# Kernel tuning notes

Measured on AMD Instinct MI355X. Metric: run time of the kernel, lower is better.

Reference implementation:

```python
import jax, jax.numpy as jnp
import numpy as np

N, E = 50000, 400000
DIN, H, EATTR, OUT = 128, 256, 8, 2
BN_EPS = 1e-5


def setup_inputs() -> dict:
    key = jax.random.key(0)
    ks = iter(jax.random.split(key, 64))
    def w(shape, scale=0.05):
        return (jax.random.normal(next(ks), shape, dtype=jnp.float32) * scale)
    inp = {
        "x": jax.random.normal(next(ks), (N, DIN), dtype=jnp.float32),
        "edge_index": jax.random.randint(next(ks), (2, E), 0, N, dtype=jnp.int32),
        "edge_attr": jax.random.normal(next(ks), (E, EATTR), dtype=jnp.float32),
    }
    # two GCN branches, 3 layers each
    dims = [(DIN, H), (H, H), (H, H)]
    for br in (1, 2):
        for li, (di, do) in enumerate(dims, start=1):
            inp[f"W{br}{li}"] = w((di, do))
            inp[f"b{br}{li}"] = jnp.zeros((do,), jnp.float32)
    # shared batchnorms
    for li in (1, 2, 3):
        inp[f"g{li}"] = jnp.ones((H,), jnp.float32)
        inp[f"be{li}"] = jnp.zeros((H,), jnp.float32)
    # edge classifier MLP: 2H+EATTR -> H -> H -> H//2 -> H//4 -> OUT
    cdims = [(2 * H + EATTR, H), (H, H), (H, H // 2), (H // 2, H // 4), (H // 4, OUT)]
    for li, (di, do) in enumerate(cdims, start=1):
        inp[f"Wc{li}"] = w((di, do))
        inp[f"bc{li}"] = jnp.zeros((do,), jnp.float32)
    return inp


def _gcn(h, W, b, src, dst, inv_sqrt_deg, n):
    # PyG GCNConv: x' = D^-1/2 (A + I) D^-1/2 (x W) + b, deg includes self-loop
    hw = h @ W                                    # [N, out]
    norm = inv_sqrt_deg[src] * inv_sqrt_deg[dst]  # [E]
    agg = jax.ops.segment_sum(hw[src] * norm[:, None], dst, num_segments=n)
    agg = agg + hw * (inv_sqrt_deg ** 2)[:, None]  # self-loop contribution
    return agg + b


def _bn_relu(h, g, b):
    m = h.mean(0)
    v = h.var(0)  # biased, as torch BN training-mode normalization
    return jax.nn.relu(g * (h - m) * jax.lax.rsqrt(v + BN_EPS) + b)


def reference(x, edge_index, edge_attr,
              W11, b11, W12, b12, W13, b13,
              W21, b21, W22, b22, W23, b23,
              g1, be1, g2, be2, g3, be3,
              Wc1, bc1, Wc2, bc2, Wc3, bc3, Wc4, bc4, Wc5, bc5):
    n = x.shape[0]
    src, dst = edge_index[0], edge_index[1]
    deg = 1.0 + jax.ops.segment_sum(jnp.ones(src.shape, x.dtype), dst, num_segments=n)
    isd = deg ** -0.5

    def branch(Ws, bs):
        h = x
        for (W, b, g, be) in zip(Ws, bs, (g1, g2, g3), (be1, be2, be3)):
            h = _gcn(h, W, b, src, dst, isd, n)
            h = _bn_relu(h, g, be)  # dropout = identity (eval)
        return h

    h1 = branch((W11, W12, W13), (b11, b12, b13))
    h2 = branch((W21, W22, W23), (b21, b22, b23))
    hc = h1 + h2

    ef = jnp.concatenate([hc[src], hc[dst], edge_attr], axis=1)  # [E, 2H+EATTR]
    h = jax.nn.relu(ef @ Wc1 + bc1)
    h = jax.nn.relu(h @ Wc2 + bc2)
    h = jax.nn.relu(h @ Wc3 + bc3)
    h = jax.nn.relu(h @ Wc4 + bc4)
    return h @ Wc5 + bc5  # [E, OUT]
```

## Files before the change

### kernel.cpp

```cpp
#include <hip/hip_runtime.h>

#define N_NODES 50000
#define N_EDGES 400000
#define EPB     128
#define NB_SCAN 196
#define BN_EPS  1e-5f
#define STAT_BLOCKS 128

typedef __attribute__((ext_vector_type(8))) short s16x8;
typedef __attribute__((ext_vector_type(4))) float f32x4;

__device__ __forceinline__ unsigned short f2bf(float x) {
    unsigned u = __float_as_uint(x);
    return (unsigned short)((u + 0x7fffu + ((u >> 16) & 1u)) >> 16);
}
__device__ __forceinline__ float bf2f(unsigned short b) {
    return __uint_as_float(((unsigned)b) << 16);
}

__device__ __forceinline__ void gload_lds16(const void* g, void* lds) {
    auto gp = reinterpret_cast<const __attribute__((address_space(1))) unsigned int*>(
        reinterpret_cast<uintptr_t>(g));
    auto lp = reinterpret_cast<__attribute__((address_space(3))) unsigned int*>(
        reinterpret_cast<uintptr_t>(lds));
    __builtin_amdgcn_global_load_lds(gp, lp, 16, 0, 0);
}

__global__ void zero_i32(int* p, int n) {
    int i = blockIdx.x * blockDim.x + threadIdx.x;
    if (i < n) p[i] = 0;
}
__global__ void zero_f32(float* p, int n) {
    int i = blockIdx.x * blockDim.x + threadIdx.x;
    if (i < n) p[i] = 0.0f;
}
__global__ void count_deg(const int* __restrict__ dst, int* __restrict__ counts) {
    int e = blockIdx.x * blockDim.x + threadIdx.x;
    if (e < N_EDGES) atomicAdd(&counts[dst[e]], 1);
}
__global__ void isd_kernel(const int* __restrict__ counts, float* __restrict__ isd) {
    int i = blockIdx.x * blockDim.x + threadIdx.x;
    if (i < N_NODES) isd[i] = rsqrtf(1.0f + (float)counts[i]);
}

__global__ __launch_bounds__(256) void scan_reduce(const int* __restrict__ counts,
                                                   int* __restrict__ bsum) {
    __shared__ int sh[256];
    int t = threadIdx.x, b = blockIdx.x;
    int i = b * 256 + t;
    sh[t] = (i < N_NODES) ? counts[i] : 0;
    __syncthreads();
    for (int o = 128; o > 0; o >>= 1) {
        if (t < o) sh[t] += sh[t + o];
        __syncthreads();
    }
    if (t == 0) bsum[b] = sh[0];
}
__global__ __launch_bounds__(256) void scan_tops(const int* __restrict__ bsum,
                                                 int* __restrict__ boff, int nb,
                                                 int* __restrict__ total_out) {
    __shared__ int sh[256];
    int t = threadIdx.x;
    int v = (t < nb) ? bsum[t] : 0;
    sh[t] = v;
    __syncthreads();
    for (int o = 1; o < 256; o <<= 1) {
        int a = (t >= o) ? sh[t - o] : 0;
        __syncthreads();
        sh[t] += a;
        __syncthreads();
    }
    if (t < nb) boff[t] = sh[t] - v;
    if (t == 255) *total_out = sh[255];
}
__global__ __launch_bounds__(256) void scan_final(const int* __restrict__ counts,
                                                  const int* __restrict__ boff,
                                                  int* __restrict__ offsets) {
    __shared__ int sh[256];
    int t = threadIdx.x, b = blockIdx.x;
    int i = b * 256 + t;
    int v = (i < N_NODES) ? counts[i] : 0;
    sh[t] = v;
    __syncthreads();
    for (int o = 1; o < 256; o <<= 1) {
        int a = (t >= o) ? sh[t - o] : 0;
        __syncthreads();
        sh[t] += a;
        __syncthreads();
    }
    if (i < N_NODES) offsets[i] = boff[b] + sh[t] - v;
}

__global__ void fill_csr(const int* __restrict__ src, const int* __restrict__ dst,
                         const float* __restrict__ isd, const int* __restrict__ offsets,
                         int* __restrict__ cursor, int2* __restrict__ pk,
                         int* __restrict__ edstA, int* __restrict__ eorigA) {
    int e = blockIdx.x * blockDim.x + threadIdx.x;
    if (e >= N_EDGES) return;
    int s = src[e], d = dst[e];
    int pos = offsets[d] + atomicAdd(&cursor[d], 1);
    pk[pos] = make_int2(s, __float_as_int(isd[s] * isd[d]));
    edstA[pos] = d;
    eorigA[pos] = e;
}

__global__ void conv_f32_bf16(const float* __restrict__ in, unsigned short* __restrict__ out,
                              int n4) {
    int i = blockIdx.x * blockDim.x + threadIdx.x;
    if (i >= n4) return;
    float4 v = ((const float4*)in)[i];
    unsigned short o0 = f2bf(v.x), o1 = f2bf(v.y), o2 = f2bf(v.z), o3 = f2bf(v.w);
    ((uint2*)out)[i] = make_uint2(((unsigned)o1 << 16) | o0, ((unsigned)o3 << 16) | o2);
}

struct WPack {
    const float* src[11];
    unsigned short* dst[11];
};
__global__ __launch_bounds__(256) void prep_weights(WPack p) {
    const int Ks[11] = {128, 128, 256, 256, 256, 256, 256, 256, 256, 256, 128};
    const int Ns[11] = {256, 256, 256, 256, 256, 256, 256, 256, 256, 128, 64};
    int seg = blockIdx.y;
    int K = Ks[seg], N = Ns[seg];
    int idx = blockIdx.x * 256 + threadIdx.x;
    if (idx >= K * N) return;
    int k = idx / N, n = idx % N;
    p.dst[seg][(size_t)n * K + k] = f2bf(p.src[seg][idx]);
}

template <int BN_T, int OUT_MODE, int RELU, int BIAS, int DUAL>
__global__ __launch_bounds__(256) void gemm_mfma(const unsigned short* __restrict__ A, int lda,
                                                 const unsigned short* __restrict__ Wt,
                                                 const float* __restrict__ bias,
                                                 void* __restrict__ Cout, int ldc,
                                                 int M, int K,
                                                 const unsigned short* __restrict__ A2,
                                                 const unsigned short* __restrict__ Wt2) {
    constexpr int MI = (BN_T == 128) ? 4 : 2;
    constexpr int NI = 4;
    __shared__ __align__(16) short As[128 * 32];
    __shared__ __align__(16) short Bs[BN_T * 32];

    const int tid = threadIdx.x;
    const int l = tid & 63;
    const int wv = tid >> 6;
    const int wrow = (BN_T == 128) ? (wv >> 1) * 64 : wv * 32;
    const int wcol = (BN_T == 128) ? (wv & 1) * 64 : 0;
    const int bm = blockIdx.x * 128;
    int bn, coloff;
    const unsigned short* Ause;
    const unsigned short* Wuse;
    if (DUAL) {
        int half_ = blockIdx.y >> 1;
        bn = (blockIdx.y & 1) * BN_T;
        coloff = half_ * 256;
        Ause = half_ ? A2 : A;
        Wuse = half_ ? Wt2 : Wt;
    } else {
        bn = blockIdx.y * BN_T;
        coloff = 0;
        Ause = A;
        Wuse = Wt;
    }
    const int rsub = l >> 2;
    const int gl = l & 3;

    f32x4 acc[MI][NI] = {};

    for (int k0 = 0; k0 < K; k0 += 32) {
#pragma unroll
        for (int i = 0; i < 2; i++) {
            int lr = wv * 32 + i * 16 + rsub;
            int gr = bm + lr;
            if (gr >= M) gr = M - 1;
            int gsrc = gl ^ ((lr >> 1) & 3);
            gload_lds16(&Ause[(size_t)gr * lda + k0 + gsrc * 8],
                        &As[(wv * 32 + i * 16) * 32]);
        }
#pragma unroll
        for (int i = 0; i < BN_T / 64; i++) {
            int base = (BN_T == 128) ? (wv * 32 + i * 16) : (wv * 16);
            int lr = base + rsub;
            int gsrc = gl ^ ((lr >> 1) & 3);
            gload_lds16(&Wuse[(size_t)(bn + lr) * K + k0 + gsrc * 8],
                        &Bs[base * 32]);
        }
        __syncthreads();

        s16x8 af[MI], bfr[NI];
        const int q = l >> 4;
#pragma unroll
        for (int mi = 0; mi < MI; mi++) {
            int r = wrow + mi * 16 + (l & 15);
            af[mi] = *(const s16x8*)(&As[r * 32 + ((q ^ ((r >> 1) & 3)) << 3)]);
        }
#pragma unroll
        for (int ni = 0; ni < NI; ni++) {
            int r = wcol + ni * 16 + (l & 15);
            bfr[ni] = *(const s16x8*)(&Bs[r * 32 + ((q ^ ((r >> 1) & 3)) << 3)]);
        }
#pragma unroll
        for (int mi = 0; mi < MI; mi++)
#pragma unroll
            for (int ni = 0; ni < NI; ni++)
                acc[mi][ni] = __builtin_amdgcn_mfma_f32_16x16x32_bf16(af[mi], bfr[ni],
                                                                      acc[mi][ni], 0, 0, 0);
        __syncthreads();
    }

#pragma unroll
    for (int mi = 0; mi < MI; mi++) {
#pragma unroll
        for (int ni = 0; ni < NI; ni++) {
            int colB = coloff + bn + wcol + ni * 16 + (l & 15);
            float bv = BIAS ? bias[colB] : 0.0f;
#pragma unroll
            for (int r = 0; r < 4; r++) {
                int row = bm + wrow + mi * 16 + (l >> 4) * 4 + r;
                if (row < M) {
                    float v = acc[mi][ni][r] + bv;
                    if (RELU) v = fmaxf(v, 0.0f);
                    if (OUT_MODE == 1)
                        ((unsigned short*)Cout)[(size_t)row * ldc + colB] = f2bf(v);
                    else
                        ((float*)Cout)[(size_t)row * ldc + colB] = v;
                }
            }
        }
    }
}

__global__ __launch_bounds__(512, 4) void edge_mlp_fused(
    const unsigned short* __restrict__ PQ, const int2* __restrict__ pk,
    const int* __restrict__ edstA, const int* __restrict__ eorigA,
    const float* __restrict__ ea, const float* __restrict__ Wc1e,
    const float* __restrict__ bc1,
    const unsigned short* __restrict__ Wc2t, const float* __restrict__ bc2,
    const unsigned short* __restrict__ Wc3t, const float* __restrict__ bc3,
    const unsigned short* __restrict__ Wc4t, const float* __restrict__ bc4,
    const float* __restrict__ Wc5, const float* __restrict__ bc5,
    float* __restrict__ out) {
    __shared__ __align__(16) short At[EPB * 256];
    __shared__ __align__(16) short Bs[256 * 32];

    const int tid = threadIdx.x;
    const int l = tid & 63;
    const int wv = tid >> 6;
    const int p0 = blockIdx.x * EPB;
    const int lm = l & 15;
    const int q = l >> 4;
    const int rsub = l >> 2;
    const int gl = l & 3;

    {
        const int c0 = l * 4;
        float bi0 = bc1[c0], bi1 = bc1[c0 + 1], bi2 = bc1[c0 + 2], bi3 = bc1[c0 + 3];
        float4 w8[8];
#pragma unroll
        for (int jj = 0; jj < 8; jj++) w8[jj] = *(const float4*)(&Wc1e[jj * 256 + c0]);
        const int g = l >> 1;
        const int sub = (l & 1) * 4;
#pragma unroll 4
        for (int i = 0; i < 16; i++) {
            int row = wv * 16 + i;
            int p = p0 + row;
            int s = pk[p].x;
            int d = edstA[p];
            int eo = eorigA[p];
            union { int2 v; unsigned short u[4]; } Pu, Qu;
            Pu.v = *(const int2*)(&PQ[(size_t)s * 512 + c0]);
            Qu.v = *(const int2*)(&PQ[(size_t)d * 512 + 256 + c0]);
            float v0 = bf2f(Pu.u[0]) + bf2f(Qu.u[0]) + bi0;
            float v1 = bf2f(Pu.u[1]) + bf2f(Qu.u[1]) + bi1;
            float v2 = bf2f(Pu.u[2]) + bf2f(Qu.u[2]) + bi2;
            float v3 = bf2f(Pu.u[3]) + bf2f(Qu.u[3]) + bi3;
#pragma unroll
            for (int jj = 0; jj < 8; jj++) {
                float av = ea[(size_t)eo * 8 + jj];
                v0 = fmaf(av, w8[jj].x, v0);
                v1 = fmaf(av, w8[jj].y, v1);
                v2 = fmaf(av, w8[jj].z, v2);
                v3 = fmaf(av, w8[jj].w, v3);
            }
            unsigned short o0 = f2bf(fmaxf(v0, 0.0f)), o1 = f2bf(fmaxf(v1, 0.0f));
            unsigned short o2 = f2bf(fmaxf(v2, 0.0f)), o3 = f2bf(fmaxf(v3, 0.0f));
            int off = row * 256 + ((g ^ (row & 7)) << 3) + sub;
            *(uint2*)(&At[off]) =
                make_uint2(((unsigned)o1 << 16) | o0, ((unsigned)o3 << 16) | o2);
        }
    }
    __syncthreads();

    {
        const int wrow = (wv >> 2) * 64;
        const int wcol = (wv & 3) * 64;
        f32x4 acc[4][4] = {};
        for (int k0 = 0; k0 < 256; k0 += 32) {
#pragma unroll
            for (int i = 0; i < 2; i++) {
                int lr = wv * 32 + i * 16 + rsub;
                int gsrc = gl ^ ((lr >> 1) & 3);
                gload_lds16(&Wc2t[(size_t)lr * 256 + k0 + gsrc * 8],
                            &Bs[(wv * 32 + i * 16) * 32]);
            }
            __syncthreads();
            s16x8 af[4], bfr[4];
#pragma unroll
            for (int mi = 0; mi < 4; mi++) {
                int r = wrow + mi * 16 + lm;
                int G = (k0 >> 3) + q;
                af[mi] = *(const s16x8*)(&At[r * 256 + ((G ^ (r & 7)) << 3)]);
            }
#pragma unroll
            for (int ni = 0; ni < 4; ni++) {
                int rb = wcol + ni * 16 + lm;
                bfr[ni] = *(const s16x8*)(&Bs[rb * 32 + ((q ^ ((rb >> 1) & 3)) << 3)]);
            }
#pragma unroll
            for (int mi = 0; mi < 4; mi++)
#pragma unroll
                for (int ni = 0; ni < 4; ni++)
                    acc[mi][ni] = __builtin_amdgcn_mfma_f32_16x16x32_bf16(
                        af[mi], bfr[ni], acc[mi][ni], 0, 0, 0);
            __syncthreads();
        }
#pragma unroll
        for (int mi = 0; mi < 4; mi++) {
#pragma unroll
            for (int ni = 0; ni < 4; ni++) {
                int col = wcol + ni * 16 + lm;
                float bv = bc2[col];
#pragma unroll
                for (int r = 0; r < 4; r++) {
                    int row = wrow + mi * 16 + q * 4 + r;
                    At[row * 256 + (((col >> 3) ^ (row & 7)) << 3) + (col & 7)] =
                        (short)f2bf(fmaxf(acc[mi][ni][r] + bv, 0.0f));
                }
            }
        }
    }
    __syncthreads();

    {
        const int wrow = (wv >> 1) * 32;
        const int wcol = (wv & 1) * 64;
        f32x4 acc[2][4] = {};
        for (int k0 = 0; k0 < 256; k0 += 32) {
            {
                int lr = wv * 16 + rsub;
                int gsrc = gl ^ ((lr >> 1) & 3);
                gload_lds16(&Wc3t[(size_t)lr * 256 + k0 + gsrc * 8],
                            &Bs[(wv * 16) * 32]);
            }
            __syncthreads();
            s16x8 af[2], bfr[4];
#pragma unroll
            for (int mi = 0; mi < 2; mi++) {
                int r = wrow + mi * 16 + lm;
                int G = (k0 >> 3) + q;
                af[mi] = *(const s16x8*)(&At[r * 256 + ((G ^ (r & 7)) << 3)]);
            }
#pragma unroll
            for (int ni = 0; ni < 4; ni++) {
                int rb = wcol + ni * 16 + lm;
                bfr[ni] = *(const s16x8*)(&Bs[rb * 32 + ((q ^ ((rb >> 1) & 3)) << 3)]);
            }
#pragma unroll
            for (int mi = 0; mi < 2; mi++)
#pragma unroll
                for (int ni = 0; ni < 4; ni++)
                    acc[mi][ni] = __builtin_amdgcn_mfma_f32_16x16x32_bf16(
                        af[mi], bfr[ni], acc[mi][ni], 0, 0, 0);
            __syncthreads();
        }
#pragma unroll
        for (int mi = 0; mi < 2; mi++) {
#pragma unroll
            for (int ni = 0; ni < 4; ni++) {
                int col = wcol + ni * 16 + lm;
                float bv = bc3[col];
#pragma unroll
                for (int r = 0; r < 4; r++) {
                    int row = wrow + mi * 16 + q * 4 + r;
                    At[row * 128 + (((col >> 3) ^ (row & 7)) << 3) + (col & 7)] =
                        (short)f2bf(fmaxf(acc[mi][ni][r] + bv, 0.0f));
                }
            }
        }
    }
    __syncthreads();

    {
        const int wrow = wv * 16;
        f32x4 acc[4] = {};
        for (int k0 = 0; k0 < 128; k0 += 32) {
            if (wv < 4) {
                int lr = wv * 16 + rsub;
                int gsrc = gl ^ ((lr >> 1) & 3);
                gload_lds16(&Wc4t[(size_t)lr * 128 + k0 + gsrc * 8],
                            &Bs[(wv * 16) * 32]);
            }
            __syncthreads();
            s16x8 af, bfr[4];
            {
                int r = wrow + lm;
                int G = (k0 >> 3) + q;
                af = *(const s16x8*)(&At[r * 128 + ((G ^ (r & 7)) << 3)]);
            }
#pragma unroll
            for (int ni = 0; ni < 4; ni++) {
                int rb = ni * 16 + lm;
                bfr[ni] = *(const s16x8*)(&Bs[rb * 32 + ((q ^ ((rb >> 1) & 3)) << 3)]);
            }
#pragma unroll
            for (int ni = 0; ni < 4; ni++)
                acc[ni] = __builtin_amdgcn_mfma_f32_16x16x32_bf16(af, bfr[ni],
                                                                  acc[ni], 0, 0, 0);
            __syncthreads();
        }
#pragma unroll
        for (int r = 0; r < 4; r++) {
            float pa = 0.f, pb = 0.f;
#pragma unroll
            for (int ni = 0; ni < 4; ni++) {
                int col = ni * 16 + lm;
                float v = fmaxf(acc[ni][r] + bc4[col], 0.0f);
                pa = fmaf(v, Wc5[col * 2 + 0], pa);
                pb = fmaf(v, Wc5[col * 2 + 1], pb);
            }
#pragma unroll
            for (int o = 1; o < 16; o <<= 1) {
                pa += __shfl_xor(pa, o, 64);
                pb += __shfl_xor(pb, o, 64);
            }
            if (lm == 0) {
                int row = wrow + q * 4 + r;
                int eo = eorigA[p0 + row];
                out[(size_t)eo * 2 + 0] = pa + bc5[0];
                out[(size_t)eo * 2 + 1] = pb + bc5[1];
            }
        }
    }
}

__global__ __launch_bounds__(256) void aggregate2(const unsigned short* __restrict__ hwb,
                                                  const float* __restrict__ isd,
                                                  const int* __restrict__ offsets,
                                                  const int2* __restrict__ pk,
                                                  const float* __restrict__ b1,
                                                  const float* __restrict__ b2,
                                                  unsigned short* __restrict__ hagg) {
    int wv = threadIdx.x >> 6, l = threadIdx.x & 63;
    int n = blockIdx.x * 4 + wv;
    int c0 = l * 8;
    float acc[8] = {};
    int e0 = offsets[n], e1 = offsets[n + 1];
    int k = e0;
    for (; k + 2 <= e1; k += 2) {
        int2 p0 = pk[k], p1 = pk[k + 1];
        union { int4 v; unsigned short u[8]; } U0, U1;
        U0.v = *(const int4*)(&hwb[(size_t)p0.x * 512 + c0]);
        U1.v = *(const int4*)(&hwb[(size_t)p1.x * 512 + c0]);
        float w0 = __int_as_float(p0.y), w1 = __int_as_float(p1.y);
#pragma unroll
        for (int j = 0; j < 8; j++)
            acc[j] = fmaf(w0, bf2f(U0.u[j]), fmaf(w1, bf2f(U1.u[j]), acc[j]));
    }
    if (k < e1) {
        int2 p0 = pk[k];
        union { int4 v; unsigned short u[8]; } U0;
        U0.v = *(const int4*)(&hwb[(size_t)p0.x * 512 + c0]);
        float w0 = __int_as_float(p0.y);
#pragma unroll
        for (int j = 0; j < 8; j++) acc[j] = fmaf(w0, bf2f(U0.u[j]), acc[j]);
    }
    float si = isd[n]; si *= si;
    union { int4 v; unsigned short u[8]; } U;
    U.v = *(const int4*)(&hwb[(size_t)n * 512 + c0]);
    const float* bp = (c0 < 256) ? (b1 + c0) : (b2 + (c0 - 256));
    unsigned short os[8];
#pragma unroll
    for (int j = 0; j < 8; j++) {
        acc[j] = fmaf(si, bf2f(U.u[j]), acc[j]) + bp[j];
        os[j] = f2bf(acc[j]);
    }
    int4 ov;
    ov.x = (int)(((unsigned)os[1] << 16) | os[0]);
    ov.y = (int)(((unsigned)os[3] << 16) | os[2]);
    ov.z = (int)(((unsigned)os[5] << 16) | os[4]);
    ov.w = (int)(((unsigned)os[7] << 16) | os[6]);
    *(int4*)(&hagg[(size_t)n * 512 + c0]) = ov;
}

__global__ __launch_bounds__(256) void bn_stats2(const unsigned short* __restrict__ h,
                                                 float* __restrict__ stats) {
    __shared__ float sh[4][1024];
    int t = threadIdx.x;
    int wv = t >> 6, l = t & 63;
    int c0 = l * 8;
    float s[8] = {}, q[8] = {};
    for (int n = blockIdx.x * 4 + wv; n < N_NODES; n += STAT_BLOCKS * 4) {
        union { int4 v; unsigned short u[8]; } U;
        U.v = *(const int4*)(&h[(size_t)n * 512 + c0]);
#pragma unroll
        for (int j = 0; j < 8; j++) {
            float x = bf2f(U.u[j]);
            s[j] += x;
            q[j] = fmaf(x, x, q[j]);
        }
    }
#pragma unroll
    for (int j = 0; j < 8; j++) {
        sh[wv][c0 + j] = s[j];
        sh[wv][512 + c0 + j] = q[j];
    }
    __syncthreads();
    for (int i = t; i < 1024; i += 256) {
        float a = sh[0][i] + sh[1][i] + sh[2][i] + sh[3][i];
        atomicAdd(&stats[i], a);
    }
}

__global__ __launch_bounds__(256) void bn_ab(const float* __restrict__ stats,
                                             const float* __restrict__ g,
                                             const float* __restrict__ be,
                                             float* __restrict__ AB,
                                             float* __restrict__ stats_mut) {
    int t = threadIdx.x;
#pragma unroll
    for (int h = 0; h < 2; h++) {
        int c = t + h * 256;
        float m = stats[c] * (1.0f / N_NODES);
        float var = stats[512 + c] * (1.0f / N_NODES) - m * m;
        float sc = g[c & 255] * rsqrtf(var + BN_EPS);
        AB[c] = sc;
        AB[512 + c] = be[c & 255] - m * sc;
        stats_mut[c] = 0.0f;
        stats_mut[512 + c] = 0.0f;
    }
}

__global__ __launch_bounds__(256) void bn_apply(const unsigned short* __restrict__ h,
                                                const float* __restrict__ AB,
                                                unsigned short* __restrict__ outp) {
    int i8 = blockIdx.x * blockDim.x + threadIdx.x;
    if (i8 >= N_NODES * 512 / 8) return;
    int c8 = (i8 & 63) * 8;
    union { int4 v; unsigned short u[8]; } U;
    U.v = *(const int4*)(&h[(size_t)i8 * 8]);
    unsigned short os[8];
#pragma unroll
    for (int j = 0; j < 8; j++) {
        int c = c8 + j;
        float y = fmaf(bf2f(U.u[j]), AB[c], AB[512 + c]);
        os[j] = f2bf(fmaxf(y, 0.0f));
    }
    int4 ov;
    ov.x = (int)(((unsigned)os[1] << 16) | os[0]);
    ov.y = (int)(((unsigned)os[3] << 16) | os[2]);
    ov.z = (int)(((unsigned)os[5] << 16) | os[4]);
    ov.w = (int)(((unsigned)os[7] << 16) | os[6]);
    *(int4*)(&outp[(size_t)i8 * 8]) = ov;
}

__global__ __launch_bounds__(256) void bn_apply_final(const unsigned short* __restrict__ h,
                                                      const float* __restrict__ AB,
                                                      unsigned short* __restrict__ hc) {
    int i8 = blockIdx.x * blockDim.x + threadIdx.x;
    if (i8 >= N_NODES * 256 / 8) return;
    int n = i8 >> 5;
    int c8 = (i8 & 31) * 8;
    union { int4 v; unsigned short u[8]; } U1, U2;
    U1.v = *(const int4*)(&h[(size_t)n * 512 + c8]);
    U2.v = *(const int4*)(&h[(size_t)n * 512 + 256 + c8]);
    unsigned short os[8];
#pragma unroll
    for (int j = 0; j < 8; j++) {
        int c = c8 + j;
        float y1 = fmaxf(fmaf(bf2f(U1.u[j]), AB[c], AB[512 + c]), 0.0f);
        int c2 = c + 256;
        float y2 = fmaxf(fmaf(bf2f(U2.u[j]), AB[c2], AB[512 + c2]), 0.0f);
        os[j] = f2bf(y1 + y2);
    }
    int4 ov;
    ov.x = (int)(((unsigned)os[1] << 16) | os[0]);
    ov.y = (int)(((unsigned)os[3] << 16) | os[2]);
    ov.z = (int)(((unsigned)os[5] << 16) | os[4]);
    ov.w = (int)(((unsigned)os[7] << 16) | os[6]);
    *(int4*)(&hc[(size_t)i8 * 8]) = ov;
}

extern "C" void kernel_launch(void* const* d_in, const int* in_sizes, int n_in,
                              void* d_out, int out_size, void* d_ws, size_t ws_size,
                              hipStream_t stream) {
    const float* x   = (const float*)d_in[0];
    const int*   ei  = (const int*)d_in[1];
    const float* ea  = (const float*)d_in[2];
    const float* W11 = (const float*)d_in[3];
    const float* b11 = (const float*)d_in[4];
    const float* W12 = (const float*)d_in[5];
    const float* b12 = (const float*)d_in[6];
    const float* W13 = (const float*)d_in[7];
    const float* b13 = (const float*)d_in[8];
    const float* W21 = (const float*)d_in[9];
    const float* b21 = (const float*)d_in[10];
    const float* W22 = (const float*)d_in[11];
    const float* b22 = (const float*)d_in[12];
    const float* W23 = (const float*)d_in[13];
    const float* b23 = (const float*)d_in[14];
    const float* g1  = (const float*)d_in[15];
    const float* be1 = (const float*)d_in[16];
    const float* g2  = (const float*)d_in[17];
    const float* be2 = (const float*)d_in[18];
    const float* g3  = (const float*)d_in[19];
    const float* be3 = (const float*)d_in[20];
    const float* Wc1 = (const float*)d_in[21];
    const float* bc1 = (const float*)d_in[22];
    const float* Wc2 = (const float*)d_in[23];
    const float* bc2 = (const float*)d_in[24];
    const float* Wc3 = (const float*)d_in[25];
    const float* bc3 = (const float*)d_in[26];
    const float* Wc4 = (const float*)d_in[27];
    const float* bc4 = (const float*)d_in[28];
    const float* Wc5 = (const float*)d_in[29];
    const float* bc5 = (const float*)d_in[30];

    const int* src = ei;
    const int* dst = ei + N_EDGES;
    float* out = (float*)d_out;

    char* w = (char*)d_ws;
    auto alloc = [&](size_t bytes) {
        char* p = w;
        w += (bytes + 255) & ~(size_t)255;
        return p;
    };
    float* isd     = (float*)alloc(N_NODES * 4);
    int2*  pk      = (int2*)alloc((size_t)N_EDGES * 8);
    int*   edstA   = (int*)alloc((size_t)N_EDGES * 4);
    int*   eorigA  = (int*)alloc((size_t)N_EDGES * 4);
    int*   counts  = (int*)alloc((N_NODES + 4) * 4);
    int*   offsets = (int*)alloc((N_NODES + 4) * 4);
    int*   bsum    = (int*)alloc(256 * 4);
    int*   boff    = (int*)alloc(256 * 4);
    float* stats   = (float*)alloc(1024 * 4);
    float* AB      = (float*)alloc(1024 * 4);
    unsigned short* W11t = (unsigned short*)alloc(256 * 128 * 2);
    unsigned short* W21t = (unsigned short*)alloc(256 * 128 * 2);
    unsigned short* W12t = (unsigned short*)alloc(256 * 256 * 2);
    unsigned short* W22t = (unsigned short*)alloc(256 * 256 * 2);
    unsigned short* W13t = (unsigned short*)alloc(256 * 256 * 2);
    unsigned short* W23t = (unsigned short*)alloc(256 * 256 * 2);
    unsigned short* WPQt = (unsigned short*)alloc(512 * 256 * 2);
    unsigned short* Wc2t = (unsigned short*)alloc(256 * 256 * 2);
    unsigned short* Wc3t = (unsigned short*)alloc(128 * 256 * 2);
    unsigned short* Wc4t = (unsigned short*)alloc(64 * 128 * 2);
    unsigned short* xb   = (unsigned short*)alloc((size_t)N_NODES * 128 * 2);
    unsigned short* hb   = (unsigned short*)alloc((size_t)N_NODES * 512 * 2);
    unsigned short* hwb  = (unsigned short*)alloc((size_t)N_NODES * 512 * 2);
    unsigned short* hagg = (unsigned short*)alloc((size_t)N_NODES * 512 * 2);
    unsigned short* hc   = (unsigned short*)alloc((size_t)N_NODES * 256 * 2);
    (void)ws_size;

    zero_i32<<<(N_NODES + 256) / 256, 256, 0, stream>>>(counts, N_NODES + 1);
    count_deg<<<(N_EDGES + 255) / 256, 256, 0, stream>>>(dst, counts);
    isd_kernel<<<(N_NODES + 255) / 256, 256, 0, stream>>>(counts, isd);
    scan_reduce<<<NB_SCAN, 256, 0, stream>>>(counts, bsum);
    scan_tops<<<1, 256, 0, stream>>>(bsum, boff, NB_SCAN, offsets + N_NODES);
    scan_final<<<NB_SCAN, 256, 0, stream>>>(counts, boff, offsets);
    zero_i32<<<(N_NODES + 255) / 256, 256, 0, stream>>>(counts, N_NODES);
    fill_csr<<<(N_EDGES + 255) / 256, 256, 0, stream>>>(src, dst, isd, offsets, counts,
                                                        pk, edstA, eorigA);

    conv_f32_bf16<<<(N_NODES * 128 / 4 + 255) / 256, 256, 0, stream>>>(x, xb,
                                                                        N_NODES * 128 / 4);
    WPack wp;
    wp.src[0] = W11; wp.dst[0] = W11t;
    wp.src[1] = W21; wp.dst[1] = W21t;
    wp.src[2] = W12; wp.dst[2] = W12t;
    wp.src[3] = W22; wp.dst[3] = W22t;
    wp.src[4] = W13; wp.dst[4] = W13t;
    wp.src[5] = W23; wp.dst[5] = W23t;
    wp.src[6] = Wc1; wp.dst[6] = WPQt;
    wp.src[7] = Wc1 + 256 * 256; wp.dst[7] = WPQt + 256 * 256;
    wp.src[8] = Wc2; wp.dst[8] = Wc2t;
    wp.src[9] = Wc3; wp.dst[9] = Wc3t;
    wp.src[10] = Wc4; wp.dst[10] = Wc4t;
    prep_weights<<<dim3(256, 11), 256, 0, stream>>>(wp);

    zero_f32<<<4, 256, 0, stream>>>(stats, 1024);

    const unsigned short* Wat[3] = {W11t, W12t, W13t};
    const unsigned short* Wbt[3] = {W21t, W22t, W23t};
    const float* ba[3] = {b11, b12, b13};
    const float* bb[3] = {b21, b22, b23};
    const float* gs[3] = {g1, g2, g3};
    const float* bes[3] = {be1, be2, be3};

    int gx_n = (N_NODES + 127) / 128;
    for (int l = 0; l < 3; l++) {
        if (l == 0) {
            gemm_mfma<128, 1, 0, 0, 1><<<dim3(gx_n, 4), 256, 0, stream>>>(
                xb, 128, Wat[0], nullptr, hwb, 512, N_NODES, 128, xb, Wbt[0]);
        } else {
            gemm_mfma<128, 1, 0, 0, 1><<<dim3(gx_n, 4), 256, 0, stream>>>(
                hb, 512, Wat[l], nullptr, hwb, 512, N_NODES, 256, hb + 256, Wbt[l]);
        }
        aggregate2<<<N_NODES / 4, 256, 0, stream>>>(hwb, isd, offsets, pk,
                                                    ba[l], bb[l], hagg);
        bn_stats2<<<STAT_BLOCKS, 256, 0, stream>>>(hagg, stats);
        bn_ab<<<1, 256, 0, stream>>>(stats, gs[l], bes[l], AB, stats);
        if (l < 2) {
            bn_apply<<<(N_NODES * 512 / 8 + 255) / 256, 256, 0, stream>>>(hagg, AB, hb);
        } else {
            bn_apply_final<<<(N_NODES * 256 / 8 + 255) / 256, 256, 0, stream>>>(hagg, AB, hc);
        }
    }

    gemm_mfma<128, 1, 0, 0, 0><<<dim3(gx_n, 4), 256, 0, stream>>>(hc, 256, WPQt, nullptr,
                                                                  hwb, 512, N_NODES, 256,
                                                                  nullptr, nullptr);

    edge_mlp_fused<<<N_EDGES / EPB, 512, 0, stream>>>(
        hwb, pk, edstA, eorigA, ea, Wc1 + 512 * 256, bc1,
        Wc2t, bc2, Wc3t, bc3, Wc4t, bc4, Wc5, bc5, out);
}
```

Before: 744.5 us.

## Aggregate first layer on 128-wide input before GEMM, shared by both branches

```diff
diff --git a/kernel.cpp b/kernel.cpp
--- a/kernel.cpp
+++ b/kernel.cpp
@@ -135,7 +135,8 @@
                                                  void* __restrict__ Cout, int ldc,
                                                  int M, int K,
                                                  const unsigned short* __restrict__ A2,
-                                                 const unsigned short* __restrict__ Wt2) {
+                                                 const unsigned short* __restrict__ Wt2,
+                                                 const float* __restrict__ bias2) {
     constexpr int MI = (BN_T == 128) ? 4 : 2;
     constexpr int NI = 4;
     __shared__ __align__(16) short As[128 * 32];
@@ -148,10 +149,11 @@
     const int wcol = (BN_T == 128) ? (wv & 1) * 64 : 0;
     const int bm = blockIdx.x * 128;
     int bn, coloff;
+    int half_ = 0;
     const unsigned short* Ause;
     const unsigned short* Wuse;
     if (DUAL) {
-        int half_ = blockIdx.y >> 1;
+        half_ = blockIdx.y >> 1;
         bn = (blockIdx.y & 1) * BN_T;
         coloff = half_ * 256;
         Ause = half_ ? A2 : A;
@@ -212,8 +214,17 @@
     for (int mi = 0; mi < MI; mi++) {
 #pragma unroll
         for (int ni = 0; ni < NI; ni++) {
-            int colB = coloff + bn + wcol + ni * 16 + (l & 15);
-            float bv = BIAS ? bias[colB] : 0.0f;
+            int colL = bn + wcol + ni * 16 + (l & 15);
+            int colB = coloff + colL;
+            float bv = 0.0f;
+            if (BIAS) {
+                if (DUAL) {
+                    const float* bp = half_ ? bias2 : bias;
+                    bv = bp[colL];
+                } else {
+                    bv = bias[colB];
+                }
+            }
 #pragma unroll
             for (int r = 0; r < 4; r++) {
                 int row = bm + wrow + mi * 16 + (l >> 4) * 4 + r;
@@ -490,6 +501,40 @@
     ov.z = (int)(((unsigned)os[5] << 16) | os[4]);
     ov.w = (int)(((unsigned)os[7] << 16) | os[6]);
     *(int4*)(&hagg[(size_t)n * 512 + c0]) = ov;
+}
+
+__global__ __launch_bounds__(256) void aggregate128(const unsigned short* __restrict__ xb,
+                                                    const float* __restrict__ isd,
+                                                    const int* __restrict__ offsets,
+                                                    const int2* __restrict__ pk,
+                                                    unsigned short* __restrict__ hagg0) {
+    int wv = threadIdx.x >> 6, l = threadIdx.x & 63;
+    int n = blockIdx.x * 4 + wv;
+    int c0 = l * 2;
+    float a0 = 0.f, a1 = 0.f;
+    int e0 = offsets[n], e1 = offsets[n + 1];
+    int k = e0;
+    for (; k + 2 <= e1; k += 2) {
+        int2 p0 = pk[k], p1 = pk[k + 1];
+        unsigned u0 = *(const unsigned*)(&xb[(size_t)p0.x * 128 + c0]);
+        unsigned u1 = *(const unsigned*)(&xb[(size_t)p1.x * 128 + c0]);
+        float w0 = __int_as_float(p0.y), w1 = __int_as_float(p1.y);
+        a0 = fmaf(w0, bf2f((unsigned short)u0), fmaf(w1, bf2f((unsigned short)u1), a0));
+        a1 = fmaf(w0, bf2f((unsigned short)(u0 >> 16)),
+                  fmaf(w1, bf2f((unsigned short)(u1 >> 16)), a1));
+    }
+    if (k < e1) {
+        int2 p0 = pk[k];
+        unsigned u0 = *(const unsigned*)(&xb[(size_t)p0.x * 128 + c0]);
+        float w0 = __int_as_float(p0.y);
+        a0 = fmaf(w0, bf2f((unsigned short)u0), a0);
+        a1 = fmaf(w0, bf2f((unsigned short)(u0 >> 16)), a1);
+    }
+    float si = isd[n]; si *= si;
+    unsigned u = *(const unsigned*)(&xb[(size_t)n * 128 + c0]);
+    a0 = fmaf(si, bf2f((unsigned short)u), a0);
+    a1 = fmaf(si, bf2f((unsigned short)(u >> 16)), a1);
+    *(unsigned*)(&hagg0[(size_t)n * 128 + c0]) = ((unsigned)f2bf(a1) << 16) | f2bf(a0);
 }
 
 __global__ __launch_bounds__(256) void bn_stats2(const unsigned short* __restrict__ h,
@@ -656,6 +701,7 @@
     unsigned short* Wc3t = (unsigned short*)alloc(128 * 256 * 2);
     unsigned short* Wc4t = (unsigned short*)alloc(64 * 128 * 2);
     unsigned short* xb   = (unsigned short*)alloc((size_t)N_NODES * 128 * 2);
+    unsigned short* hagg0 = (unsigned short*)alloc((size_t)N_NODES * 128 * 2);
     unsigned short* hb   = (unsigned short*)alloc((size_t)N_NODES * 512 * 2);
     unsigned short* hwb  = (unsigned short*)alloc((size_t)N_NODES * 512 * 2);
     unsigned short* hagg = (unsigned short*)alloc((size_t)N_NODES * 512 * 2);
@@ -690,6 +736,15 @@
 
     zero_f32<<<4, 256, 0, stream>>>(stats, 1024);
 
+    int gx_n = (N_NODES + 127) / 128;
+
+    aggregate128<<<N_NODES / 4, 256, 0, stream>>>(xb, isd, offsets, pk, hagg0);
+    gemm_mfma<128, 1, 0, 1, 1><<<dim3(gx_n, 4), 256, 0, stream>>>(
+        hagg0, 128, W11t, b11, hwb, 512, N_NODES, 128, hagg0, W21t, b21);
+    bn_stats2<<<STAT_BLOCKS, 256, 0, stream>>>(hwb, stats);
+    bn_ab<<<1, 256, 0, stream>>>(stats, g1, be1, AB, stats);
+    bn_apply<<<(N_NODES * 512 / 8 + 255) / 256, 256, 0, stream>>>(hwb, AB, hb);
+
     const unsigned short* Wat[3] = {W11t, W12t, W13t};
     const unsigned short* Wbt[3] = {W21t, W22t, W23t};
     const float* ba[3] = {b11, b12, b13};
@@ -697,15 +752,9 @@
     const float* gs[3] = {g1, g2, g3};
     const float* bes[3] = {be1, be2, be3};
 
-    int gx_n = (N_NODES + 127) / 128;
-    for (int l = 0; l < 3; l++) {
-        if (l == 0) {
-            gemm_mfma<128, 1, 0, 0, 1><<<dim3(gx_n, 4), 256, 0, stream>>>(
-                xb, 128, Wat[0], nullptr, hwb, 512, N_NODES, 128, xb, Wbt[0]);
-        } else {
-            gemm_mfma<128, 1, 0, 0, 1><<<dim3(gx_n, 4), 256, 0, stream>>>(
-                hb, 512, Wat[l], nullptr, hwb, 512, N_NODES, 256, hb + 256, Wbt[l]);
-        }
+    for (int l = 1; l < 3; l++) {
+        gemm_mfma<128, 1, 0, 0, 1><<<dim3(gx_n, 4), 256, 0, stream>>>(
+            hb, 512, Wat[l], nullptr, hwb, 512, N_NODES, 256, hb + 256, Wbt[l], nullptr);
         aggregate2<<<N_NODES / 4, 256, 0, stream>>>(hwb, isd, offsets, pk,
                                                     ba[l], bb[l], hagg);
         bn_stats2<<<STAT_BLOCKS, 256, 0, stream>>>(hagg, stats);
@@ -719,7 +768,7 @@
 
     gemm_mfma<128, 1, 0, 0, 0><<<dim3(gx_n, 4), 256, 0, stream>>>(hc, 256, WPQt, nullptr,
                                                                   hwb, 512, N_NODES, 256,
-                                                                  nullptr, nullptr);
+                                                                  nullptr, nullptr, nullptr);
 
     edge_mlp_fused<<<N_EDGES / EPB, 512, 0, stream>>>(
         hwb, pk, edstA, eorigA, ea, Wc1 + 512 * 256, bc1,
```

After: 730.9 us. No clear change (-1.8%).
